# Optimization experiments

Hardware: AMD Instinct MI355X
Metric: run time of the kernel (lower is better)

## Reference

```python
import jax, jax.numpy as jnp
import numpy as np

TOP_K = 2

def _sparse_moe(x, gate_w, w1, w2, w3):
    # x: [b, S, D] -> per-token top-k routed SwiGLU experts (Mixtral style)
    D = x.shape[-1]
    E = gate_w.shape[1]
    t = x.reshape(-1, D)                      # [T, D] tokens
    logits = t @ gate_w                       # [T, E]
    probs = jax.nn.softmax(logits, axis=-1)
    topw, topi = jax.lax.top_k(probs, TOP_K)  # [T, k]
    topw = topw / jnp.sum(topw, axis=-1, keepdims=True)
    out = jnp.zeros_like(t)
    for e in range(E):  # small fixed expert loop
        w_e = jnp.sum(jnp.where(topi == e, topw, 0.0), axis=-1)  # [T]
        h = jax.nn.silu(t @ w1[e]) * (t @ w3[e])                 # [T, F]
        out = out + (h @ w2[e]) * w_e[:, None]
    return out.reshape(x.shape)

def setup_inputs() -> dict:
    key = jax.random.key(0)
    ks = jax.random.split(key, 5)
    B, S, D, F, E = 4, 512, 1024, 4096, 8
    sc = 0.02
    return {
        "data": jax.random.normal(ks[0], (B, S, D), jnp.float32),
        "gate_w": jax.random.normal(ks[1], (D, E), jnp.float32) * sc,
        "w1": jax.random.normal(ks[2], (E, D, F), jnp.float32) * sc,
        "w2": jax.random.normal(ks[3], (E, F, D), jnp.float32) * sc,
        "w3": jax.random.normal(ks[4], (E, D, F), jnp.float32) * sc,
    }

def reference(data, gate_w, w1, w2, w3):
    # FeedForward._mixlora_forward: slice batch per lora config, run MoE,
    # combine with index_add_ (disjoint ranges covering the batch).
    B = data.shape[0]
    splits = [(0, B // 2), (B // 2, B)]  # two lora_batch_data_config_ entries
    final = jnp.zeros_like(data)
    for s, e in splits:
        y = _sparse_moe(data[s:e], gate_w, w1, w2, w3)
        final = final.at[jnp.arange(s, e)].add(y)  # index_add_ combine
    return final
```

## Files before the change

### kernel.cpp

```cpp
#include <hip/hip_runtime.h>
#include <hip/hip_bf16.h>
#include <math.h>

#define D_DIM 1024
#define F_DIM 4096
#define N_EXP 8

typedef __attribute__((ext_vector_type(4))) float f32x4;
typedef __attribute__((ext_vector_type(8))) short bf16x8;

__device__ __forceinline__ unsigned short f2bf(float f) {
    union { float f; unsigned int u; } v; v.f = f;
    unsigned int r = v.u + 0x7fffu + ((v.u >> 16) & 1u);
    return (unsigned short)(r >> 16);
}

#define GLDS16(g, l) __builtin_amdgcn_global_load_lds( \
    (const __attribute__((address_space(1))) void*)(g), \
    (__attribute__((address_space(3))) void*)(l), 16, 0, 0)

#define WAIT4_BAR asm volatile("s_waitcnt vmcnt(4)\ns_barrier" ::: "memory")
#define WAIT3_BAR asm volatile("s_waitcnt vmcnt(3)\ns_barrier" ::: "memory")
#define BAR       asm volatile("s_barrier" ::: "memory")

__global__ void cast_x_kernel(const float* __restrict__ x, unsigned short* __restrict__ xb, int n4) {
    int i = blockIdx.x * blockDim.x + threadIdx.x;
    if (i >= n4) return;
    float4 v = ((const float4*)x)[i];
    unsigned int lo = (unsigned int)f2bf(v.x) | ((unsigned int)f2bf(v.y) << 16);
    unsigned int hi = (unsigned int)f2bf(v.z) | ((unsigned int)f2bf(v.w) << 16);
    ((uint2*)xb)[i] = make_uint2(lo, hi);
}

__global__ __launch_bounds__(256) void transpose_cast_kernel(
    const float* __restrict__ in, unsigned short* __restrict__ out, int R, int C) {
    __shared__ float tile[64][65];
    const float* inp = in + (size_t)blockIdx.z * R * C;
    unsigned short* outp = out + (size_t)blockIdx.z * R * C;
    int r0 = blockIdx.y * 64, c0 = blockIdx.x * 64;
    int tid = threadIdx.x;
    int tr = tid >> 4, tc = (tid & 15) * 4;
#pragma unroll
    for (int i = 0; i < 4; i++) {
        float4 v = *(const float4*)(inp + (size_t)(r0 + tr + i * 16) * C + c0 + tc);
        tile[tr + i * 16][tc + 0] = v.x;
        tile[tr + i * 16][tc + 1] = v.y;
        tile[tr + i * 16][tc + 2] = v.z;
        tile[tr + i * 16][tc + 3] = v.w;
    }
    __syncthreads();
    int wc = tid >> 4, wr = (tid & 15) * 4;
#pragma unroll
    for (int i = 0; i < 4; i++) {
        int c = wc + i * 16;
        ushort4 o;
        o.x = f2bf(tile[wr + 0][c]);
        o.y = f2bf(tile[wr + 1][c]);
        o.z = f2bf(tile[wr + 2][c]);
        o.w = f2bf(tile[wr + 3][c]);
        *(ushort4*)(outp + (size_t)(c0 + c) * R + r0 + wr) = o;
    }
}

__global__ void gate_kernel(const float* __restrict__ x, const float* __restrict__ gw,
                            int* __restrict__ counts, int* __restrict__ perm,
                            float* __restrict__ wts, int* __restrict__ islot, int T) {
    int wid = threadIdx.x >> 6, lane = threadIdx.x & 63;
    int token = blockIdx.x * 4 + wid;
    if (token >= T) return;
    float acc[N_EXP];
#pragma unroll
    for (int e = 0; e < N_EXP; e++) acc[e] = 0.f;
    const float* xr = x + (size_t)token * D_DIM;
    for (int i = 0; i < D_DIM / 64; i++) {
        int d = lane + 64 * i;
        float v = xr[d];
#pragma unroll
        for (int e = 0; e < N_EXP; e++) acc[e] += v * gw[d * N_EXP + e];
    }
#pragma unroll
    for (int off = 32; off >= 1; off >>= 1) {
#pragma unroll
        for (int e = 0; e < N_EXP; e++) acc[e] += __shfl_xor(acc[e], off, 64);
    }
    if (lane == 0) {
        float m = acc[0];
#pragma unroll
        for (int e = 1; e < N_EXP; e++) m = fmaxf(m, acc[e]);
        float p[N_EXP];
#pragma unroll
        for (int e = 0; e < N_EXP; e++) p[e] = expf(acc[e] - m);
        int a = 0;
        for (int e = 1; e < N_EXP; e++) if (p[e] > p[a]) a = e;
        int b = (a == 0) ? 1 : 0;
        for (int e = 0; e < N_EXP; e++) if (e != a && p[e] > p[b]) b = e;
        float s = p[a] + p[b];
        int pa = atomicAdd(&counts[a], 1);
        perm[(size_t)a * T + pa] = token; wts[(size_t)a * T + pa] = p[a] / s;
        int pb = atomicAdd(&counts[b], 1);
        perm[(size_t)b * T + pb] = token; wts[(size_t)b * T + pb] = p[b] / s;
        islot[2 * token + 0] = a * T + pa;
        islot[2 * token + 1] = b * T + pb;
    }
}

__global__ void offsets_kernel(const int* __restrict__ counts, int* __restrict__ offs) {
    if (threadIdx.x == 0 && blockIdx.x == 0) {
        int s = 0;
        for (int e = 0; e < N_EXP; e++) { offs[e] = s; s += counts[e]; }
        offs[N_EXP] = s;
    }
}

__global__ __launch_bounds__(256, 4) void gemm1_kernel(
    const unsigned short* __restrict__ xb, const unsigned short* __restrict__ w1t,
    const unsigned short* __restrict__ w3t, const int* __restrict__ counts,
    const int* __restrict__ offs, const int* __restrict__ perm,
    unsigned short* __restrict__ hbuf, int T)
{
    int bid = blockIdx.x;
    int s  = bid & 7;
    int rt = (bid >> 3) & 15;
    int ce = ((bid >> 7) << 3) | s;
    int e  = ce & 7;
    int ct = ce >> 3;
    int n_e = counts[e];
    int row0 = rt * 128;
    if (row0 >= n_e) return;
    int c0 = ct * 64;
    const unsigned short* w1e = w1t + (size_t)e * F_DIM * D_DIM;
    const unsigned short* w3e = w3t + (size_t)e * F_DIM * D_DIM;
    __shared__ unsigned short As0[4096], As1[4096];
    __shared__ unsigned short B10[2048], B11[2048];
    __shared__ unsigned short B30[2048], B31[2048];
    int tid = threadIdx.x;
    int wid = tid >> 6, lane = tid & 63;
    int wm = wid >> 1, wn = wid & 1;
    int q = lane >> 4, ln = lane & 15;

    int sr = tid >> 2, sc = tid & 3;
    int q0 = sc ^ ((sr >> 1) & 3);
    int tok0 = perm[(size_t)e * T + min(row0 + sr, n_e - 1)];
    int tok1 = perm[(size_t)e * T + min(row0 + sr + 64, n_e - 1)];
    const unsigned short* ag0 = xb + (size_t)tok0 * D_DIM + q0 * 8;
    const unsigned short* ag1 = xb + (size_t)tok1 * D_DIM + q0 * 8;
    const unsigned short* b1g = w1e + (size_t)(c0 + sr) * D_DIM + q0 * 8;
    const unsigned short* b3g = w3e + (size_t)(c0 + sr) * D_DIM + q0 * 8;
    int wo = wid * 512;

    int a_off[4], b_off[2];
#pragma unroll
    for (int i = 0; i < 4; i++) {
        int m = wm * 64 + i * 16 + ln;
        a_off[i] = m * 32 + (q ^ ((m >> 1) & 3)) * 8;
    }
#pragma unroll
    for (int j = 0; j < 2; j++) {
        int n = wn * 32 + j * 16 + ln;
        b_off[j] = n * 32 + (q ^ ((n >> 1) & 3)) * 8;
    }

    f32x4 acc1[4][2], acc3[4][2];
#pragma unroll
    for (int i = 0; i < 4; i++)
#pragma unroll
        for (int j = 0; j < 2; j++) {
            acc1[i][j] = (f32x4){0.f, 0.f, 0.f, 0.f};
            acc3[i][j] = (f32x4){0.f, 0.f, 0.f, 0.f};
        }

#define ISSUE1(AS, B1S, B3S, K) do { \
    GLDS16(ag0 + (K), &AS[wo]); \
    GLDS16(ag1 + (K), &AS[wo + 2048]); \
    GLDS16(b1g + (K), &B1S[wo]); \
    GLDS16(b3g + (K), &B3S[wo]); } while (0)

#define COMPUTE1(AS, B1S, B3S) do { \
    bf16x8 af[4]; \
    _Pragma("unroll") for (int i = 0; i < 4; i++) af[i] = *(const bf16x8*)&AS[a_off[i]]; \
    _Pragma("unroll") for (int j = 0; j < 2; j++) { \
        bf16x8 b1f = *(const bf16x8*)&B1S[b_off[j]]; \
        bf16x8 b3f = *(const bf16x8*)&B3S[b_off[j]]; \
        _Pragma("unroll") for (int i = 0; i < 4; i++) { \
            acc1[i][j] = __builtin_amdgcn_mfma_f32_16x16x32_bf16(af[i], b1f, acc1[i][j], 0, 0, 0); \
            acc3[i][j] = __builtin_amdgcn_mfma_f32_16x16x32_bf16(af[i], b3f, acc3[i][j], 0, 0, 0); \
        } \
    } } while (0)

    ISSUE1(As0, B10, B30, 0);
    for (int it = 0; it < 32; it += 2) {
        int kn1 = (it + 1) * 32;
        ISSUE1(As1, B11, B31, kn1);
        WAIT4_BAR;
        COMPUTE1(As0, B10, B30);
        BAR;
        int kn2 = (it + 2 < 32) ? (it + 2) * 32 : 0;
        ISSUE1(As0, B10, B30, kn2);
        WAIT4_BAR;
        COMPUTE1(As1, B11, B31);
        BAR;
    }

    int hb = offs[e];
#pragma unroll
    for (int i = 0; i < 4; i++) {
#pragma unroll
        for (int r = 0; r < 4; r++) {
            int grow = row0 + wm * 64 + i * 16 + q * 4 + r;
            if (grow < n_e) {
                size_t hrow = (size_t)(hb + grow) * F_DIM;
#pragma unroll
                for (int j = 0; j < 2; j++) {
                    int col = c0 + wn * 32 + j * 16 + ln;
                    float p1 = acc1[i][j][r];
                    float p3 = acc3[i][j][r];
                    float h = (p1 / (1.f + expf(-p1))) * p3;
                    hbuf[hrow + col] = f2bf(h);
                }
            }
        }
    }
}

__global__ __launch_bounds__(256, 4) void gemm2_kernel(
    const unsigned short* __restrict__ hbuf, const unsigned short* __restrict__ w2t,
    const int* __restrict__ counts, const int* __restrict__ offs,
    const float* __restrict__ wts, float* __restrict__ obuf, int T)
{
    int bid = blockIdx.x;
    int s  = bid & 7;
    int rt = (bid >> 3) & 15;
    int ce = ((bid >> 7) << 3) | s;
    int e  = ce & 7;
    int ct = ce >> 3;
    int n_e = counts[e];
    int row0 = rt * 128;
    if (row0 >= n_e) return;
    int c0 = ct * 64;
    const unsigned short* w2e = w2t + (size_t)e * D_DIM * F_DIM;
    __shared__ unsigned short As0[4096], As1[4096];
    __shared__ unsigned short Bs0[2048], Bs1[2048];
    int tid = threadIdx.x;
    int wid = tid >> 6, lane = tid & 63;
    int wm = wid >> 1, wn = wid & 1;
    int q = lane >> 4, ln = lane & 15;
    int hb = offs[e];

    int sr = tid >> 2, sc = tid & 3;
    int q0 = sc ^ ((sr >> 1) & 3);
    int ar0 = hb + min(row0 + sr, n_e - 1);
    int ar1 = hb + min(row0 + sr + 64, n_e - 1);
    const unsigned short* ag0 = hbuf + (size_t)ar0 * F_DIM + q0 * 8;
    const unsigned short* ag1 = hbuf + (size_t)ar1 * F_DIM + q0 * 8;
    const unsigned short* bg  = w2e + (size_t)(c0 + sr) * F_DIM + q0 * 8;
    int wo = wid * 512;

    int a_off[4], b_off[2];
#pragma unroll
    for (int i = 0; i < 4; i++) {
        int m = wm * 64 + i * 16 + ln;
        a_off[i] = m * 32 + (q ^ ((m >> 1) & 3)) * 8;
    }
#pragma unroll
    for (int j = 0; j < 2; j++) {
        int n = wn * 32 + j * 16 + ln;
        b_off[j] = n * 32 + (q ^ ((n >> 1) & 3)) * 8;
    }

    f32x4 acc[4][2];
#pragma unroll
    for (int i = 0; i < 4; i++)
#pragma unroll
        for (int j = 0; j < 2; j++) acc[i][j] = (f32x4){0.f, 0.f, 0.f, 0.f};

#define ISSUE2(AS, BS, K) do { \
    GLDS16(ag0 + (K), &AS[wo]); \
    GLDS16(ag1 + (K), &AS[wo + 2048]); \
    GLDS16(bg + (K), &BS[wo]); } while (0)

#define COMPUTE2(AS, BS) do { \
    bf16x8 af[4]; \
    _Pragma("unroll") for (int i = 0; i < 4; i++) af[i] = *(const bf16x8*)&AS[a_off[i]]; \
    _Pragma("unroll") for (int j = 0; j < 2; j++) { \
        bf16x8 bf = *(const bf16x8*)&BS[b_off[j]]; \
        _Pragma("unroll") for (int i = 0; i < 4; i++) \
            acc[i][j] = __builtin_amdgcn_mfma_f32_16x16x32_bf16(af[i], bf, acc[i][j], 0, 0, 0); \
    } } while (0)

    ISSUE2(As0, Bs0, 0);
    for (int it = 0; it < 128; it += 2) {
        int kn1 = (it + 1) * 32;
        ISSUE2(As1, Bs1, kn1);
        WAIT3_BAR;
        COMPUTE2(As0, Bs0);
        BAR;
        int kn2 = (it + 2 < 128) ? (it + 2) * 32 : 0;
        ISSUE2(As0, Bs0, kn2);
        WAIT3_BAR;
        COMPUTE2(As1, Bs1);
        BAR;
    }

#pragma unroll
    for (int i = 0; i < 4; i++) {
#pragma unroll
        for (int r = 0; r < 4; r++) {
            int grow = row0 + wm * 64 + i * 16 + q * 4 + r;
            if (grow < n_e) {
                float w = wts[(size_t)e * T + grow];
                float* orow = obuf + (size_t)(hb + grow) * D_DIM;
#pragma unroll
                for (int j = 0; j < 2; j++) {
                    int col = c0 + wn * 32 + j * 16 + ln;
                    orow[col] = acc[i][j][r] * w;
                }
            }
        }
    }
}

__global__ void combine_kernel(const float* __restrict__ obuf, const int* __restrict__ islot,
                               const int* __restrict__ offs, float* __restrict__ out, int T) {
    int idx = blockIdx.x * 256 + threadIdx.x;
    int n4 = T * (D_DIM / 4);
    if (idx >= n4) return;
    int t = idx / (D_DIM / 4);
    int c4 = idx - t * (D_DIM / 4);
    int v0 = islot[2 * t], v1 = islot[2 * t + 1];
    int e0 = v0 / T, e1 = v1 / T;
    int s0 = offs[e0] + (v0 - e0 * T);
    int s1 = offs[e1] + (v1 - e1 * T);
    float4 a = ((const float4*)obuf)[(size_t)s0 * (D_DIM / 4) + c4];
    float4 b = ((const float4*)obuf)[(size_t)s1 * (D_DIM / 4) + c4];
    float4 o; o.x = a.x + b.x; o.y = a.y + b.y; o.z = a.z + b.z; o.w = a.w + b.w;
    ((float4*)out)[idx] = o;
}

extern "C" void kernel_launch(void* const* d_in, const int* in_sizes, int n_in,
                              void* d_out, int out_size, void* d_ws, size_t ws_size,
                              hipStream_t stream) {
    const float* x  = (const float*)d_in[0];
    const float* gw = (const float*)d_in[1];
    const float* w1 = (const float*)d_in[2];
    const float* w2 = (const float*)d_in[3];
    const float* w3 = (const float*)d_in[4];
    float* out = (float*)d_out;
    int T = in_sizes[0] / D_DIM;

    char* ws = (char*)d_ws;
    size_t off = 0;
    unsigned short* xb = (unsigned short*)(ws + off); off += (size_t)T * D_DIM * 2;
    int* counts = (int*)(ws + off); off += 256;
    int* offs   = (int*)(ws + off); off += 256;
    int* perm   = (int*)(ws + off); off += (size_t)N_EXP * T * 4;
    float* wts  = (float*)(ws + off); off += (size_t)N_EXP * T * 4;
    int* islot  = (int*)(ws + off); off += (size_t)2 * T * 4;
    unsigned short* hbuf = (unsigned short*)(ws + off); off += (size_t)2 * T * F_DIM * 2;
    unsigned short* w1t  = (unsigned short*)(ws + off); off += (size_t)N_EXP * D_DIM * F_DIM * 2;
    unsigned short* w3t  = (unsigned short*)(ws + off); off += (size_t)N_EXP * D_DIM * F_DIM * 2;
    unsigned short* w2t  = w1t;
    float* obuf = (float*)w3t;

    hipMemsetAsync(counts, 0, 256, stream);

    int n4 = T * D_DIM / 4;
    cast_x_kernel<<<(n4 + 255) / 256, 256, 0, stream>>>(x, xb, n4);
    gate_kernel<<<T / 4, 256, 0, stream>>>(x, gw, counts, perm, wts, islot, T);
    offsets_kernel<<<1, 64, 0, stream>>>(counts, offs);

    dim3 gt13(F_DIM / 64, D_DIM / 64, N_EXP);
    transpose_cast_kernel<<<gt13, 256, 0, stream>>>(w1, w1t, D_DIM, F_DIM);
    transpose_cast_kernel<<<gt13, 256, 0, stream>>>(w3, w3t, D_DIM, F_DIM);

    gemm1_kernel<<<(F_DIM / 64) * N_EXP * 16, 256, 0, stream>>>(
        xb, w1t, w3t, counts, offs, perm, hbuf, T);

    dim3 gt2(D_DIM / 64, F_DIM / 64, N_EXP);
    transpose_cast_kernel<<<gt2, 256, 0, stream>>>(w2, w2t, F_DIM, D_DIM);

    gemm2_kernel<<<(D_DIM / 64) * N_EXP * 16, 256, 0, stream>>>(
        hbuf, w2t, counts, offs, wts, obuf, T);

    combine_kernel<<<(T * D_DIM / 4 + 255) / 256, 256, 0, stream>>>(obuf, islot, offs, out, T);
}
```

Measured before the change: 669.7 us.

## Deepen GEMM LDS pipeline to four stages and interleave experts in transpose grid

Both grouped GEMM kernels move from double-buffered to four-stage LDS buffering, keeping three k-tiles of global_load_lds in flight and waiting with larger vmcnt thresholds. A final drain is added after the loop. The transpose-cast grid is remapped so consecutive blocks walk different experts, which spreads concurrent memory traffic. The deeper pipeline doubles LDS use per block (to about 64KB in gemm1), which may cut how many blocks fit per CU below the four requested by the launch bounds.

```diff
diff --git a/kernel.cpp b/kernel.cpp
--- a/kernel.cpp
+++ b/kernel.cpp
@@ -19,9 +19,10 @@
     (const __attribute__((address_space(1))) void*)(g), \
     (__attribute__((address_space(3))) void*)(l), 16, 0, 0)
 
-#define WAIT4_BAR asm volatile("s_waitcnt vmcnt(4)\ns_barrier" ::: "memory")
-#define WAIT3_BAR asm volatile("s_waitcnt vmcnt(3)\ns_barrier" ::: "memory")
-#define BAR       asm volatile("s_barrier" ::: "memory")
+#define WAIT12_BAR asm volatile("s_waitcnt vmcnt(12)\ns_barrier" ::: "memory")
+#define WAIT9_BAR  asm volatile("s_waitcnt vmcnt(9)\ns_barrier" ::: "memory")
+#define BAR        asm volatile("s_barrier" ::: "memory")
+#define DRAIN      asm volatile("s_waitcnt vmcnt(0)" ::: "memory")
 
 __global__ void cast_x_kernel(const float* __restrict__ x, unsigned short* __restrict__ xb, int n4) {
     int i = blockIdx.x * blockDim.x + threadIdx.x;
@@ -35,9 +36,10 @@
 __global__ __launch_bounds__(256) void transpose_cast_kernel(
     const float* __restrict__ in, unsigned short* __restrict__ out, int R, int C) {
     __shared__ float tile[64][65];
-    const float* inp = in + (size_t)blockIdx.z * R * C;
-    unsigned short* outp = out + (size_t)blockIdx.z * R * C;
-    int r0 = blockIdx.y * 64, c0 = blockIdx.x * 64;
+    int e = blockIdx.x & 7;
+    const float* inp = in + (size_t)e * R * C;
+    unsigned short* outp = out + (size_t)e * R * C;
+    int r0 = blockIdx.y * 64, c0 = (blockIdx.x >> 3) * 64;
     int tid = threadIdx.x;
     int tr = tid >> 4, tc = (tid & 15) * 4;
 #pragma unroll
@@ -130,9 +132,9 @@
     int c0 = ct * 64;
     const unsigned short* w1e = w1t + (size_t)e * F_DIM * D_DIM;
     const unsigned short* w3e = w3t + (size_t)e * F_DIM * D_DIM;
-    __shared__ unsigned short As0[4096], As1[4096];
-    __shared__ unsigned short B10[2048], B11[2048];
-    __shared__ unsigned short B30[2048], B31[2048];
+    __shared__ __attribute__((aligned(16))) unsigned short As[4][4096];
+    __shared__ __attribute__((aligned(16))) unsigned short B1s[4][2048];
+    __shared__ __attribute__((aligned(16))) unsigned short B3s[4][2048];
     int tid = threadIdx.x;
     int wid = tid >> 6, lane = tid & 63;
     int wm = wid >> 1, wn = wid & 1;
@@ -169,37 +171,39 @@
             acc3[i][j] = (f32x4){0.f, 0.f, 0.f, 0.f};
         }
 
-#define ISSUE1(AS, B1S, B3S, K) do { \
-    GLDS16(ag0 + (K), &AS[wo]); \
-    GLDS16(ag1 + (K), &AS[wo + 2048]); \
-    GLDS16(b1g + (K), &B1S[wo]); \
-    GLDS16(b3g + (K), &B3S[wo]); } while (0)
-
-#define COMPUTE1(AS, B1S, B3S) do { \
+#define ISSUE1(B, K) do { \
+    GLDS16(ag0 + (K), &As[B][wo]); \
+    GLDS16(ag1 + (K), &As[B][wo + 2048]); \
+    GLDS16(b1g + (K), &B1s[B][wo]); \
+    GLDS16(b3g + (K), &B3s[B][wo]); } while (0)
+
+#define COMPUTE1(B) do { \
     bf16x8 af[4]; \
-    _Pragma("unroll") for (int i = 0; i < 4; i++) af[i] = *(const bf16x8*)&AS[a_off[i]]; \
+    _Pragma("unroll") for (int i = 0; i < 4; i++) af[i] = *(const bf16x8*)&As[B][a_off[i]]; \
     _Pragma("unroll") for (int j = 0; j < 2; j++) { \
-        bf16x8 b1f = *(const bf16x8*)&B1S[b_off[j]]; \
-        bf16x8 b3f = *(const bf16x8*)&B3S[b_off[j]]; \
+        bf16x8 b1f = *(const bf16x8*)&B1s[B][b_off[j]]; \
+        bf16x8 b3f = *(const bf16x8*)&B3s[B][b_off[j]]; \
         _Pragma("unroll") for (int i = 0; i < 4; i++) { \
             acc1[i][j] = __builtin_amdgcn_mfma_f32_16x16x32_bf16(af[i], b1f, acc1[i][j], 0, 0, 0); \
             acc3[i][j] = __builtin_amdgcn_mfma_f32_16x16x32_bf16(af[i], b3f, acc3[i][j], 0, 0, 0); \
         } \
     } } while (0)
 
-    ISSUE1(As0, B10, B30, 0);
-    for (int it = 0; it < 32; it += 2) {
-        int kn1 = (it + 1) * 32;
-        ISSUE1(As1, B11, B31, kn1);
-        WAIT4_BAR;
-        COMPUTE1(As0, B10, B30);
-        BAR;
-        int kn2 = (it + 2 < 32) ? (it + 2) * 32 : 0;
-        ISSUE1(As0, B10, B30, kn2);
-        WAIT4_BAR;
-        COMPUTE1(As1, B11, B31);
-        BAR;
-    }
+    ISSUE1(0, 0);
+    ISSUE1(1, 32);
+    ISSUE1(2, 64);
+    for (int it = 0; it < 32; it += 4) {
+        int k3 = it + 3, k4 = it + 4, k5 = it + 5, k6 = it + 6;
+        ISSUE1(3, (k3 < 32) ? k3 * 32 : 0);
+        WAIT12_BAR; COMPUTE1(0); BAR;
+        ISSUE1(0, (k4 < 32) ? k4 * 32 : 0);
+        WAIT12_BAR; COMPUTE1(1); BAR;
+        ISSUE1(1, (k5 < 32) ? k5 * 32 : 0);
+        WAIT12_BAR; COMPUTE1(2); BAR;
+        ISSUE1(2, (k6 < 32) ? k6 * 32 : 0);
+        WAIT12_BAR; COMPUTE1(3); BAR;
+    }
+    DRAIN;
 
     int hb = offs[e];
 #pragma unroll
@@ -238,8 +242,8 @@
     if (row0 >= n_e) return;
     int c0 = ct * 64;
     const unsigned short* w2e = w2t + (size_t)e * D_DIM * F_DIM;
-    __shared__ unsigned short As0[4096], As1[4096];
-    __shared__ unsigned short Bs0[2048], Bs1[2048];
+    __shared__ __attribute__((aligned(16))) unsigned short As[4][4096];
+    __shared__ __attribute__((aligned(16))) unsigned short Bs[4][2048];
     int tid = threadIdx.x;
     int wid = tid >> 6, lane = tid & 63;
     int wm = wid >> 1, wn = wid & 1;
@@ -273,33 +277,35 @@
 #pragma unroll
         for (int j = 0; j < 2; j++) acc[i][j] = (f32x4){0.f, 0.f, 0.f, 0.f};
 
-#define ISSUE2(AS, BS, K) do { \
-    GLDS16(ag0 + (K), &AS[wo]); \
-    GLDS16(ag1 + (K), &AS[wo + 2048]); \
-    GLDS16(bg + (K), &BS[wo]); } while (0)
-
-#define COMPUTE2(AS, BS) do { \
+#define ISSUE2(B, K) do { \
+    GLDS16(ag0 + (K), &As[B][wo]); \
+    GLDS16(ag1 + (K), &As[B][wo + 2048]); \
+    GLDS16(bg + (K), &Bs[B][wo]); } while (0)
+
+#define COMPUTE2(B) do { \
     bf16x8 af[4]; \
-    _Pragma("unroll") for (int i = 0; i < 4; i++) af[i] = *(const bf16x8*)&AS[a_off[i]]; \
+    _Pragma("unroll") for (int i = 0; i < 4; i++) af[i] = *(const bf16x8*)&As[B][a_off[i]]; \
     _Pragma("unroll") for (int j = 0; j < 2; j++) { \
-        bf16x8 bf = *(const bf16x8*)&BS[b_off[j]]; \
+        bf16x8 bf = *(const bf16x8*)&Bs[B][b_off[j]]; \
         _Pragma("unroll") for (int i = 0; i < 4; i++) \
             acc[i][j] = __builtin_amdgcn_mfma_f32_16x16x32_bf16(af[i], bf, acc[i][j], 0, 0, 0); \
     } } while (0)
 
-    ISSUE2(As0, Bs0, 0);
-    for (int it = 0; it < 128; it += 2) {
-        int kn1 = (it + 1) * 32;
-        ISSUE2(As1, Bs1, kn1);
-        WAIT3_BAR;
-        COMPUTE2(As0, Bs0);
-        BAR;
-        int kn2 = (it + 2 < 128) ? (it + 2) * 32 : 0;
-        ISSUE2(As0, Bs0, kn2);
-        WAIT3_BAR;
-        COMPUTE2(As1, Bs1);
-        BAR;
-    }
+    ISSUE2(0, 0);
+    ISSUE2(1, 32);
+    ISSUE2(2, 64);
+    for (int it = 0; it < 128; it += 4) {
+        int k3 = it + 3, k4 = it + 4, k5 = it + 5, k6 = it + 6;
+        ISSUE2(3, (k3 < 128) ? k3 * 32 : 0);
+        WAIT9_BAR; COMPUTE2(0); BAR;
+        ISSUE2(0, (k4 < 128) ? k4 * 32 : 0);
+        WAIT9_BAR; COMPUTE2(1); BAR;
+        ISSUE2(1, (k5 < 128) ? k5 * 32 : 0);
+        WAIT9_BAR; COMPUTE2(2); BAR;
+        ISSUE2(2, (k6 < 128) ? k6 * 32 : 0);
+        WAIT9_BAR; COMPUTE2(3); BAR;
+    }
+    DRAIN;
 
 #pragma unroll
     for (int i = 0; i < 4; i++) {
@@ -368,14 +374,14 @@
     gate_kernel<<<T / 4, 256, 0, stream>>>(x, gw, counts, perm, wts, islot, T);
     offsets_kernel<<<1, 64, 0, stream>>>(counts, offs);
 
-    dim3 gt13(F_DIM / 64, D_DIM / 64, N_EXP);
+    dim3 gt13((F_DIM / 64) * N_EXP, D_DIM / 64);
     transpose_cast_kernel<<<gt13, 256, 0, stream>>>(w1, w1t, D_DIM, F_DIM);
     transpose_cast_kernel<<<gt13, 256, 0, stream>>>(w3, w3t, D_DIM, F_DIM);
 
     gemm1_kernel<<<(F_DIM / 64) * N_EXP * 16, 256, 0, stream>>>(
         xb, w1t, w3t, counts, offs, perm, hbuf, T);
 
-    dim3 gt2(D_DIM / 64, F_DIM / 64, N_EXP);
+    dim3 gt2((D_DIM / 64) * N_EXP, F_DIM / 64);
     transpose_cast_kernel<<<gt2, 256, 0, stream>>>(w2, w2t, F_DIM, D_DIM);
 
     gemm2_kernel<<<(D_DIM / 64) * N_EXP * 16, 256, 0, stream>>>(
```

Measured after the change: 761.3 us. +13.7%, slower.

## Load B fragments directly to registers and interleave expert index in transpose grid

Applied to the files above, without the earlier changes.

Both expert GEMMs stop staging the weight (B) tiles through LDS. Each lane now loads its bf16x8 B fragment straight from global memory into registers, double-buffered alongside the A tiles, and the vmcnt waits are adjusted to match. This cuts LDS traffic and footprint, but each wave now issues its own uncoalesced-ish global B loads with duplication across the wm waves, and gemm1's launch bounds drop to 3 blocks per CU to leave room for the extra registers. The transpose-cast grid also interleaves the expert index into blockIdx.x, which changes the order in which blocks touch memory.

```diff
diff --git a/kernel.cpp b/kernel.cpp
--- a/kernel.cpp
+++ b/kernel.cpp
@@ -19,9 +19,10 @@
     (const __attribute__((address_space(1))) void*)(g), \
     (__attribute__((address_space(3))) void*)(l), 16, 0, 0)
 
+#define WAIT6_BAR asm volatile("s_waitcnt vmcnt(6)\ns_barrier" ::: "memory")
 #define WAIT4_BAR asm volatile("s_waitcnt vmcnt(4)\ns_barrier" ::: "memory")
-#define WAIT3_BAR asm volatile("s_waitcnt vmcnt(3)\ns_barrier" ::: "memory")
 #define BAR       asm volatile("s_barrier" ::: "memory")
+#define DRAIN     asm volatile("s_waitcnt vmcnt(0)" ::: "memory")
 
 __global__ void cast_x_kernel(const float* __restrict__ x, unsigned short* __restrict__ xb, int n4) {
     int i = blockIdx.x * blockDim.x + threadIdx.x;
@@ -35,9 +36,10 @@
 __global__ __launch_bounds__(256) void transpose_cast_kernel(
     const float* __restrict__ in, unsigned short* __restrict__ out, int R, int C) {
     __shared__ float tile[64][65];
-    const float* inp = in + (size_t)blockIdx.z * R * C;
-    unsigned short* outp = out + (size_t)blockIdx.z * R * C;
-    int r0 = blockIdx.y * 64, c0 = blockIdx.x * 64;
+    int e = blockIdx.x & 7;
+    const float* inp = in + (size_t)e * R * C;
+    unsigned short* outp = out + (size_t)e * R * C;
+    int r0 = blockIdx.y * 64, c0 = (blockIdx.x >> 3) * 64;
     int tid = threadIdx.x;
     int tr = tid >> 4, tc = (tid & 15) * 4;
 #pragma unroll
@@ -112,7 +114,7 @@
     }
 }
 
-__global__ __launch_bounds__(256, 4) void gemm1_kernel(
+__global__ __launch_bounds__(256, 3) void gemm1_kernel(
     const unsigned short* __restrict__ xb, const unsigned short* __restrict__ w1t,
     const unsigned short* __restrict__ w3t, const int* __restrict__ counts,
     const int* __restrict__ offs, const int* __restrict__ perm,
@@ -130,9 +132,7 @@
     int c0 = ct * 64;
     const unsigned short* w1e = w1t + (size_t)e * F_DIM * D_DIM;
     const unsigned short* w3e = w3t + (size_t)e * F_DIM * D_DIM;
-    __shared__ unsigned short As0[4096], As1[4096];
-    __shared__ unsigned short B10[2048], B11[2048];
-    __shared__ unsigned short B30[2048], B31[2048];
+    __shared__ __attribute__((aligned(16))) unsigned short As[2][4096];
     int tid = threadIdx.x;
     int wid = tid >> 6, lane = tid & 63;
     int wm = wid >> 1, wn = wid & 1;
@@ -144,21 +144,20 @@
     int tok1 = perm[(size_t)e * T + min(row0 + sr + 64, n_e - 1)];
     const unsigned short* ag0 = xb + (size_t)tok0 * D_DIM + q0 * 8;
     const unsigned short* ag1 = xb + (size_t)tok1 * D_DIM + q0 * 8;
-    const unsigned short* b1g = w1e + (size_t)(c0 + sr) * D_DIM + q0 * 8;
-    const unsigned short* b3g = w3e + (size_t)(c0 + sr) * D_DIM + q0 * 8;
     int wo = wid * 512;
 
-    int a_off[4], b_off[2];
+    int a_off[4];
 #pragma unroll
     for (int i = 0; i < 4; i++) {
         int m = wm * 64 + i * 16 + ln;
         a_off[i] = m * 32 + (q ^ ((m >> 1) & 3)) * 8;
     }
-#pragma unroll
-    for (int j = 0; j < 2; j++) {
-        int n = wn * 32 + j * 16 + ln;
-        b_off[j] = n * 32 + (q ^ ((n >> 1) & 3)) * 8;
-    }
+
+    int n0 = c0 + wn * 32 + ln;
+    const unsigned short* pb1_0 = w1e + (size_t)(n0     ) * D_DIM + q * 8;
+    const unsigned short* pb1_1 = w1e + (size_t)(n0 + 16) * D_DIM + q * 8;
+    const unsigned short* pb3_0 = w3e + (size_t)(n0     ) * D_DIM + q * 8;
+    const unsigned short* pb3_1 = w3e + (size_t)(n0 + 16) * D_DIM + q * 8;
 
     f32x4 acc1[4][2], acc3[4][2];
 #pragma unroll
@@ -169,37 +168,44 @@
             acc3[i][j] = (f32x4){0.f, 0.f, 0.f, 0.f};
         }
 
-#define ISSUE1(AS, B1S, B3S, K) do { \
-    GLDS16(ag0 + (K), &AS[wo]); \
-    GLDS16(ag1 + (K), &AS[wo + 2048]); \
-    GLDS16(b1g + (K), &B1S[wo]); \
-    GLDS16(b3g + (K), &B3S[wo]); } while (0)
-
-#define COMPUTE1(AS, B1S, B3S) do { \
+#define ISSUE_A1(B, K) do { \
+    GLDS16(ag0 + (K), &As[B][wo]); \
+    GLDS16(ag1 + (K), &As[B][wo + 2048]); } while (0)
+
+#define LOADB1(s0, s1, s2, s3, K) do { \
+    s0 = *(const bf16x8*)(pb1_0 + (K)); \
+    s1 = *(const bf16x8*)(pb1_1 + (K)); \
+    s2 = *(const bf16x8*)(pb3_0 + (K)); \
+    s3 = *(const bf16x8*)(pb3_1 + (K)); } while (0)
+
+#define COMPUTE1(AS, B10, B11, B30, B31) do { \
     bf16x8 af[4]; \
     _Pragma("unroll") for (int i = 0; i < 4; i++) af[i] = *(const bf16x8*)&AS[a_off[i]]; \
-    _Pragma("unroll") for (int j = 0; j < 2; j++) { \
-        bf16x8 b1f = *(const bf16x8*)&B1S[b_off[j]]; \
-        bf16x8 b3f = *(const bf16x8*)&B3S[b_off[j]]; \
-        _Pragma("unroll") for (int i = 0; i < 4; i++) { \
-            acc1[i][j] = __builtin_amdgcn_mfma_f32_16x16x32_bf16(af[i], b1f, acc1[i][j], 0, 0, 0); \
-            acc3[i][j] = __builtin_amdgcn_mfma_f32_16x16x32_bf16(af[i], b3f, acc3[i][j], 0, 0, 0); \
-        } \
+    _Pragma("unroll") for (int i = 0; i < 4; i++) { \
+        acc1[i][0] = __builtin_amdgcn_mfma_f32_16x16x32_bf16(af[i], B10, acc1[i][0], 0, 0, 0); \
+        acc3[i][0] = __builtin_amdgcn_mfma_f32_16x16x32_bf16(af[i], B30, acc3[i][0], 0, 0, 0); \
+        acc1[i][1] = __builtin_amdgcn_mfma_f32_16x16x32_bf16(af[i], B11, acc1[i][1], 0, 0, 0); \
+        acc3[i][1] = __builtin_amdgcn_mfma_f32_16x16x32_bf16(af[i], B31, acc3[i][1], 0, 0, 0); \
     } } while (0)
 
-    ISSUE1(As0, B10, B30, 0);
+    bf16x8 b1a0, b1a1, b3a0, b3a1, b1b0, b1b1, b3b0, b3b1;
+    ISSUE_A1(0, 0);
+    LOADB1(b1a0, b1a1, b3a0, b3a1, 0);
     for (int it = 0; it < 32; it += 2) {
-        int kn1 = (it + 1) * 32;
-        ISSUE1(As1, B11, B31, kn1);
-        WAIT4_BAR;
-        COMPUTE1(As0, B10, B30);
+        int k1 = (it + 1) * 32;
+        ISSUE_A1(1, k1);
+        LOADB1(b1b0, b1b1, b3b0, b3b1, k1);
+        WAIT6_BAR;
+        COMPUTE1(As[0], b1a0, b1a1, b3a0, b3a1);
         BAR;
-        int kn2 = (it + 2 < 32) ? (it + 2) * 32 : 0;
-        ISSUE1(As0, B10, B30, kn2);
-        WAIT4_BAR;
-        COMPUTE1(As1, B11, B31);
+        int k2 = (it + 2 < 32) ? (it + 2) * 32 : 0;
+        ISSUE_A1(0, k2);
+        LOADB1(b1a0, b1a1, b3a0, b3a1, k2);
+        WAIT6_BAR;
+        COMPUTE1(As[1], b1b0, b1b1, b3b0, b3b1);
         BAR;
     }
+    DRAIN;
 
     int hb = offs[e];
 #pragma unroll
@@ -238,8 +244,7 @@
     if (row0 >= n_e) return;
     int c0 = ct * 64;
     const unsigned short* w2e = w2t + (size_t)e * D_DIM * F_DIM;
-    __shared__ unsigned short As0[4096], As1[4096];
-    __shared__ unsigned short Bs0[2048], Bs1[2048];
+    __shared__ __attribute__((aligned(16))) unsigned short As[2][4096];
     int tid = threadIdx.x;
     int wid = tid >> 6, lane = tid & 63;
     int wm = wid >> 1, wn = wid & 1;
@@ -252,20 +257,18 @@
     int ar1 = hb + min(row0 + sr + 64, n_e - 1);
     const unsigned short* ag0 = hbuf + (size_t)ar0 * F_DIM + q0 * 8;
     const unsigned short* ag1 = hbuf + (size_t)ar1 * F_DIM + q0 * 8;
-    const unsigned short* bg  = w2e + (size_t)(c0 + sr) * F_DIM + q0 * 8;
     int wo = wid * 512;
 
-    int a_off[4], b_off[2];
+    int a_off[4];
 #pragma unroll
     for (int i = 0; i < 4; i++) {
         int m = wm * 64 + i * 16 + ln;
         a_off[i] = m * 32 + (q ^ ((m >> 1) & 3)) * 8;
     }
-#pragma unroll
-    for (int j = 0; j < 2; j++) {
-        int n = wn * 32 + j * 16 + ln;
-        b_off[j] = n * 32 + (q ^ ((n >> 1) & 3)) * 8;
-    }
+
+    int n0 = c0 + wn * 32 + ln;
+    const unsigned short* pb_0 = w2e + (size_t)(n0     ) * F_DIM + q * 8;
+    const unsigned short* pb_1 = w2e + (size_t)(n0 + 16) * F_DIM + q * 8;
 
     f32x4 acc[4][2];
 #pragma unroll
@@ -273,33 +276,40 @@
 #pragma unroll
         for (int j = 0; j < 2; j++) acc[i][j] = (f32x4){0.f, 0.f, 0.f, 0.f};
 
-#define ISSUE2(AS, BS, K) do { \
-    GLDS16(ag0 + (K), &AS[wo]); \
-    GLDS16(ag1 + (K), &AS[wo + 2048]); \
-    GLDS16(bg + (K), &BS[wo]); } while (0)
-
-#define COMPUTE2(AS, BS) do { \
+#define ISSUE_A2(B, K) do { \
+    GLDS16(ag0 + (K), &As[B][wo]); \
+    GLDS16(ag1 + (K), &As[B][wo + 2048]); } while (0)
+
+#define LOADB2(s0, s1, K) do { \
+    s0 = *(const bf16x8*)(pb_0 + (K)); \
+    s1 = *(const bf16x8*)(pb_1 + (K)); } while (0)
+
+#define COMPUTE2(AS, B0, B1) do { \
     bf16x8 af[4]; \
     _Pragma("unroll") for (int i = 0; i < 4; i++) af[i] = *(const bf16x8*)&AS[a_off[i]]; \
-    _Pragma("unroll") for (int j = 0; j < 2; j++) { \
-        bf16x8 bf = *(const bf16x8*)&BS[b_off[j]]; \
-        _Pragma("unroll") for (int i = 0; i < 4; i++) \
-            acc[i][j] = __builtin_amdgcn_mfma_f32_16x16x32_bf16(af[i], bf, acc[i][j], 0, 0, 0); \
+    _Pragma("unroll") for (int i = 0; i < 4; i++) { \
+        acc[i][0] = __builtin_amdgcn_mfma_f32_16x16x32_bf16(af[i], B0, acc[i][0], 0, 0, 0); \
+        acc[i][1] = __builtin_amdgcn_mfma_f32_16x16x32_bf16(af[i], B1, acc[i][1], 0, 0, 0); \
     } } while (0)
 
-    ISSUE2(As0, Bs0, 0);
+    bf16x8 ba0, ba1, bb0, bb1;
+    ISSUE_A2(0, 0);
+    LOADB2(ba0, ba1, 0);
     for (int it = 0; it < 128; it += 2) {
-        int kn1 = (it + 1) * 32;
-        ISSUE2(As1, Bs1, kn1);
-        WAIT3_BAR;
-        COMPUTE2(As0, Bs0);
+        int k1 = (it + 1) * 32;
+        ISSUE_A2(1, k1);
+        LOADB2(bb0, bb1, k1);
+        WAIT4_BAR;
+        COMPUTE2(As[0], ba0, ba1);
         BAR;
-        int kn2 = (it + 2 < 128) ? (it + 2) * 32 : 0;
-        ISSUE2(As0, Bs0, kn2);
-        WAIT3_BAR;
-        COMPUTE2(As1, Bs1);
+        int k2 = (it + 2 < 128) ? (it + 2) * 32 : 0;
+        ISSUE_A2(0, k2);
+        LOADB2(ba0, ba1, k2);
+        WAIT4_BAR;
+        COMPUTE2(As[1], bb0, bb1);
         BAR;
     }
+    DRAIN;
 
 #pragma unroll
     for (int i = 0; i < 4; i++) {
@@ -368,14 +378,14 @@
     gate_kernel<<<T / 4, 256, 0, stream>>>(x, gw, counts, perm, wts, islot, T);
     offsets_kernel<<<1, 64, 0, stream>>>(counts, offs);
 
-    dim3 gt13(F_DIM / 64, D_DIM / 64, N_EXP);
+    dim3 gt13((F_DIM / 64) * N_EXP, D_DIM / 64);
     transpose_cast_kernel<<<gt13, 256, 0, stream>>>(w1, w1t, D_DIM, F_DIM);
     transpose_cast_kernel<<<gt13, 256, 0, stream>>>(w3, w3t, D_DIM, F_DIM);
 
     gemm1_kernel<<<(F_DIM / 64) * N_EXP * 16, 256, 0, stream>>>(
         xb, w1t, w3t, counts, offs, perm, hbuf, T);
 
-    dim3 gt2(D_DIM / 64, F_DIM / 64, N_EXP);
+    dim3 gt2((D_DIM / 64) * N_EXP, F_DIM / 64);
     transpose_cast_kernel<<<gt2, 256, 0, stream>>>(w2, w2t, F_DIM, D_DIM);
 
     gemm2_kernel<<<(D_DIM / 64) * N_EXP * 16, 256, 0, stream>>>(
```

After: 927.3 us. 1.38x slower.
